# Performance work log

Measured on AMD Instinct MI355X. Metric: run time of the kernel, lower is better.

Reference implementation:

```python
import jax, jax.numpy as jnp
import numpy as np

SCALE = 0.125  # 1/sqrt(D_head=64)
NEG_INF = -1.0e9


def setup_inputs() -> dict:
    key = jax.random.key(0)
    kq, kk, kv, km = jax.random.split(key, 4)
    B, L, N, D = 2, 2048, 16, 64
    query = jax.random.normal(kq, (B, L, N, D), dtype=jnp.float32)
    k = jax.random.normal(kk, (B, L, N, D), dtype=jnp.float32)
    v = jax.random.normal(kv, (B, L, N, D), dtype=jnp.float32)
    attn_mask = jax.random.randint(km, (B, L, L), 0, 2).astype(jnp.bool_)
    return {"query": query, "key": k, "value": v, "attn_mask": attn_mask}


def reference(query, key, value, attn_mask):
    # scores: [B, L_q, L_k, N]
    attention = jnp.einsum('bind,bjnd->bijn', query, key) * SCALE
    # mask broadcast over heads; True positions are masked out
    attention = jnp.where(attn_mask[:, :, :, None], NEG_INF, attention)
    # softmax over the key axis (dim=2), dropout p=0.0 is identity
    attention = jax.nn.softmax(attention, axis=2)
    context = jnp.einsum('bijn,bjnd->bind', attention, value)
    return (context, attention)
```

## Files before the change

### kernel.cpp

```cpp
#include <hip/hip_runtime.h>
#include <hip/hip_bf16.h>

typedef unsigned short u16;
typedef unsigned char u8;
typedef __attribute__((ext_vector_type(8))) short bf16x8;
typedef __attribute__((ext_vector_type(4))) float f32x4;

#define MFMA16(a, b, c) __builtin_amdgcn_mfma_f32_16x16x32_bf16(a, b, c, 0, 0, 0)

static __device__ __forceinline__ u16 f2bf(float f) {
    __hip_bfloat16 h = __float2bfloat16(f);
    return *reinterpret_cast<u16*>(&h);
}
static __device__ __forceinline__ float bf2f(u16 h) {
    unsigned u = ((unsigned)h) << 16;
    return __uint_as_float(u);
}

__global__ __launch_bounds__(256) void kconv_kernel(const float* __restrict__ kf,
                                                    u16* __restrict__ kb) {
    const size_t i = ((size_t)blockIdx.x * 256 + threadIdx.x) * 4;
    float4 f = *(const float4*)(kf + i);
    alignas(8) u16 w[4] = {f2bf(f.x), f2bf(f.y), f2bf(f.z), f2bf(f.w)};
    *(uint2*)(kb + i) = *(const uint2*)w;
}

__global__ __launch_bounds__(256) void vt_kernel(const float* __restrict__ v,
                                                 u16* __restrict__ vt) {
    __shared__ u16 T[64][72];
    const int t = threadIdx.x, bid = blockIdx.x;
    const int b = bid >> 9, n = bid & 15, j0 = ((bid >> 4) & 31) << 6;
    {
        const int jj = t >> 4, tt = t & 15;
#pragma unroll
        for (int rep = 0; rep < 4; rep++) {
            const int j = rep * 16 + jj;
            const float* src = v + (((size_t)((b * 2048 + j0 + j) * 16 + n)) << 6) + tt * 4;
            float4 f = *(const float4*)src;
            alignas(8) u16 w[4] = {f2bf(f.x), f2bf(f.y), f2bf(f.z), f2bf(f.w)};
            *(uint2*)&T[j][tt * 4] = *(const uint2*)w;
        }
    }
    __syncthreads();
    {
        const int d = t >> 2, jq = t & 3;
        alignas(16) u16 w[16];
#pragma unroll
        for (int e = 0; e < 16; e++) w[e] = T[jq * 16 + e][d];
        u16* dst = vt + (((size_t)((b * 16 + n) * 64 + d)) << 11) + j0 + jq * 16;
        *(uint4*)dst = *(const uint4*)&w[0];
        *(uint4*)(dst + 8) = *(const uint4*)&w[8];
    }
}

__global__ __launch_bounds__(1024, 4) void attn_kernel(
    const float* __restrict__ qf, const u16* __restrict__ kb_g,
    const u16* __restrict__ vt, const void* __restrict__ mask,
    float* __restrict__ ctx, float* __restrict__ attn) {
    __shared__ u16 maskT[2048];
    __shared__ u16 pbuf[16][16][40];

    const int tid = threadIdx.x;
    const int lane = tid & 63;
    const int wv = tid >> 6;
    const int g = lane >> 4, c = lane & 15;
    const int rbit = g * 4;

    const int bid = blockIdx.x;
    const int b = ((bid & 7) < 4) ? 0 : 1;
    const int idx = ((bid >> 3) << 2) | (bid & 3);
    const int i0 = idx << 4;

    bool mask_is_u8;
    {
        unsigned acc = 0;
        const unsigned* mw = (const unsigned*)mask;
#pragma unroll
        for (int i = 0; i < 64; i++) acc |= mw[i];
        mask_is_u8 = (acc & 0xFFFFFF00u) != 0u;
    }

    {
        const size_t base = ((size_t)(b * 2048 + i0)) * 2048 + (size_t)tid * 2;
        unsigned m0 = 0, m1 = 0;
        if (mask_is_u8) {
            const u8* m8 = (const u8*)mask;
#pragma unroll
            for (int i = 0; i < 16; i++) {
                const u8* mp = m8 + base + (size_t)i * 2048;
                if (mp[0]) m0 |= (1u << i);
                if (mp[1]) m1 |= (1u << i);
            }
        } else {
            const int* m32 = (const int*)mask;
#pragma unroll
            for (int i = 0; i < 16; i++) {
                const int* mp = m32 + base + (size_t)i * 2048;
                if (mp[0]) m0 |= (1u << i);
                if (mp[1]) m1 |= (1u << i);
            }
        }
        *reinterpret_cast<unsigned*>(&maskT[tid * 2]) = m0 | (m1 << 16);
    }
    __syncthreads();

    bf16x8 aq0, aq1;
    {
        const float* qp = qf + (((size_t)(b * 2048 + i0 + c) * 16 + wv) << 6) + g * 8;
        float4 f0 = *(const float4*)qp;
        float4 f1 = *(const float4*)(qp + 4);
        float4 f2 = *(const float4*)(qp + 32);
        float4 f3 = *(const float4*)(qp + 36);
        alignas(16) u16 w0[8] = {f2bf(f0.x), f2bf(f0.y), f2bf(f0.z), f2bf(f0.w),
                                 f2bf(f1.x), f2bf(f1.y), f2bf(f1.z), f2bf(f1.w)};
        alignas(16) u16 w1[8] = {f2bf(f2.x), f2bf(f2.y), f2bf(f2.z), f2bf(f2.w),
                                 f2bf(f3.x), f2bf(f3.y), f2bf(f3.z), f2bf(f3.w)};
        aq0 = *(const bf16x8*)w0;
        aq1 = *(const bf16x8*)w1;
    }

    const u16* kb = kb_g + (((size_t)(b * 2048) * 16 + wv) << 6) + g * 8;
    const u16* vb = vt + (((size_t)(b * 16 + wv)) << 17);

    float l0 = 0.f, l1 = 0.f, l2 = 0.f, l3 = 0.f;
    for (int j0 = 0; j0 < 2048; j0 += 16) {
        const u16* kp = kb + (size_t)(j0 + c) * 1024;
        bf16x8 b0 = *(const bf16x8*)kp;
        bf16x8 b1 = *(const bf16x8*)(kp + 32);
        f32x4 s = {0.f, 0.f, 0.f, 0.f};
        s = MFMA16(aq0, b0, s);
        s = MFMA16(aq1, b1, s);
        const unsigned mt = maskT[j0 + c];
        l0 += __expf(((mt >> (rbit + 0)) & 1) ? -1e9f : s[0] * 0.125f);
        l1 += __expf(((mt >> (rbit + 1)) & 1) ? -1e9f : s[1] * 0.125f);
        l2 += __expf(((mt >> (rbit + 2)) & 1) ? -1e9f : s[2] * 0.125f);
        l3 += __expf(((mt >> (rbit + 3)) & 1) ? -1e9f : s[3] * 0.125f);
    }
#pragma unroll
    for (int off = 1; off <= 8; off <<= 1) {
        l0 += __shfl_xor(l0, off);
        l1 += __shfl_xor(l1, off);
        l2 += __shfl_xor(l2, off);
        l3 += __shfl_xor(l3, off);
    }
    const float n0i = (l0 != 0.f) ? 1.f / l0 : 0.f;
    const float n1i = (l1 != 0.f) ? 1.f / l1 : 0.f;
    const float n2i = (l2 != 0.f) ? 1.f / l2 : 0.f;
    const float n3i = (l3 != 0.f) ? 1.f / l3 : 0.f;

    f32x4 o0 = {0.f, 0.f, 0.f, 0.f}, o1 = o0, o2 = o0, o3 = o0;

    const int wo_i = tid >> 6;
    const int wo_c = tid & 63;
    const int wo_j = wo_c >> 1;
    const int wo_n = (wo_c & 1) << 3;
    float* attn_row = attn + (((size_t)(b * 2048 + i0 + wo_i)) << 15) + wo_n;

    for (int j0 = 0; j0 < 2048; j0 += 32) {
#pragma unroll
        for (int sub = 0; sub < 2; sub++) {
            const int jb = j0 + (sub << 4);
            const u16* kp = kb + (size_t)(jb + c) * 1024;
            bf16x8 b0 = *(const bf16x8*)kp;
            bf16x8 b1 = *(const bf16x8*)(kp + 32);
            f32x4 s = {0.f, 0.f, 0.f, 0.f};
            s = MFMA16(aq0, b0, s);
            s = MFMA16(aq1, b1, s);
            const unsigned mt = maskT[jb + c];
            const int jj = (sub << 4) + c;
            pbuf[wv][rbit + 0][jj] =
                f2bf(__expf(((mt >> (rbit + 0)) & 1) ? -1e9f : s[0] * 0.125f) * n0i);
            pbuf[wv][rbit + 1][jj] =
                f2bf(__expf(((mt >> (rbit + 1)) & 1) ? -1e9f : s[1] * 0.125f) * n1i);
            pbuf[wv][rbit + 2][jj] =
                f2bf(__expf(((mt >> (rbit + 2)) & 1) ? -1e9f : s[2] * 0.125f) * n2i);
            pbuf[wv][rbit + 3][jj] =
                f2bf(__expf(((mt >> (rbit + 3)) & 1) ? -1e9f : s[3] * 0.125f) * n3i);
        }
        __syncthreads();
        {
            const bf16x8 ap = *(const bf16x8*)&pbuf[wv][c][g * 8];
            const u16* vp = vb + (size_t)c * 2048 + j0 + g * 8;
            bf16x8 v0 = *(const bf16x8*)(vp);
            bf16x8 v1 = *(const bf16x8*)(vp + 16 * 2048);
            bf16x8 v2 = *(const bf16x8*)(vp + 32 * 2048);
            bf16x8 v3 = *(const bf16x8*)(vp + 48 * 2048);
            o0 = MFMA16(ap, v0, o0);
            o1 = MFMA16(ap, v1, o1);
            o2 = MFMA16(ap, v2, o2);
            o3 = MFMA16(ap, v3, o3);
        }
        {
            alignas(16) float w[8];
#pragma unroll
            for (int e = 0; e < 8; e++) w[e] = bf2f(pbuf[wo_n + e][wo_i][wo_j]);
            float* dst = attn_row + (size_t)(j0 + wo_j) * 16;
            *(float4*)dst = *(const float4*)&w[0];
            *(float4*)(dst + 4) = *(const float4*)&w[4];
        }
        __syncthreads();
    }

#pragma unroll
    for (int r = 0; r < 4; r++) {
        float* cp = ctx + (((size_t)(b * 2048 + i0 + rbit + r) * 16 + wv) << 6) + c;
        cp[0]  = o0[r];
        cp[16] = o1[r];
        cp[32] = o2[r];
        cp[48] = o3[r];
    }
}

extern "C" void kernel_launch(void* const* d_in, const int* in_sizes, int n_in,
                              void* d_out, int out_size, void* d_ws, size_t ws_size,
                              hipStream_t stream) {
    const float* q   = (const float*)d_in[0];
    const float* k   = (const float*)d_in[1];
    const float* v   = (const float*)d_in[2];
    const void* mask = (const void*)d_in[3];

    float* ctx  = (float*)d_out;
    float* attn = (float*)d_out + 4194304;

    u16* vt = (u16*)d_ws;
    u16* kb = vt + 4194304;

    kconv_kernel<<<4096, 256, 0, stream>>>(k, kb);
    vt_kernel<<<1024, 256, 0, stream>>>(v, vt);
    attn_kernel<<<256, 1024, 0, stream>>>(q, kb, vt, mask, ctx, attn);
}
```

Baseline: 979.7 us.

## Double-buffer P tile, prefetch next K/V in registers, drop second barrier

The second-pass loop now double-buffers the shared probability tile, so the trailing __syncthreads is removed and one LDS-only barrier remains per iteration. K and V fragments for the next 32-column step are loaded into registers while the current step's PV MFMAs and attention writeback run, hiding global load latency. Attention output stores become nontemporal to avoid polluting cache. It costs extra registers and LDS at 1024 threads per block, which may cause spills or lower occupancy.

Result: faster. 919.2 us (-6.2%).

```diff
diff --git a/kernel.cpp b/kernel.cpp
--- a/kernel.cpp
+++ b/kernel.cpp
@@ -7,6 +7,13 @@
 typedef __attribute__((ext_vector_type(4))) float f32x4;
 
 #define MFMA16(a, b, c) __builtin_amdgcn_mfma_f32_16x16x32_bf16(a, b, c, 0, 0, 0)
+
+#define LGKM_BARRIER()                                     \
+    do {                                                   \
+        asm volatile("s_waitcnt lgkmcnt(0)" ::: "memory"); \
+        __builtin_amdgcn_s_barrier();                      \
+        asm volatile("" ::: "memory");                     \
+    } while (0)
 
 static __device__ __forceinline__ u16 f2bf(float f) {
     __hip_bfloat16 h = __float2bfloat16(f);
@@ -58,7 +65,7 @@
     const u16* __restrict__ vt, const void* __restrict__ mask,
     float* __restrict__ ctx, float* __restrict__ attn) {
     __shared__ u16 maskT[2048];
-    __shared__ u16 pbuf[16][16][40];
+    __shared__ u16 pbuf[2][16][16][40];
 
     const int tid = threadIdx.x;
     const int lane = tid & 63;
@@ -156,49 +163,89 @@
     const int wo_n = (wo_c & 1) << 3;
     float* attn_row = attn + (((size_t)(b * 2048 + i0 + wo_i)) << 15) + wo_n;
 
-    for (int j0 = 0; j0 < 2048; j0 += 32) {
-#pragma unroll
-        for (int sub = 0; sub < 2; sub++) {
-            const int jb = j0 + (sub << 4);
-            const u16* kp = kb + (size_t)(jb + c) * 1024;
-            bf16x8 b0 = *(const bf16x8*)kp;
-            bf16x8 b1 = *(const bf16x8*)(kp + 32);
+    bf16x8 ck0a, ck0b, ck1a, ck1b, cv0, cv1, cv2, cv3;
+    {
+        const u16* kp0 = kb + (size_t)c * 1024;
+        ck0a = *(const bf16x8*)kp0;
+        ck0b = *(const bf16x8*)(kp0 + 32);
+        const u16* kp1 = kb + (size_t)(16 + c) * 1024;
+        ck1a = *(const bf16x8*)kp1;
+        ck1b = *(const bf16x8*)(kp1 + 32);
+        const u16* vp = vb + (size_t)c * 2048 + g * 8;
+        cv0 = *(const bf16x8*)(vp);
+        cv1 = *(const bf16x8*)(vp + 16 * 2048);
+        cv2 = *(const bf16x8*)(vp + 32 * 2048);
+        cv3 = *(const bf16x8*)(vp + 48 * 2048);
+    }
+
+    int p = 0;
+    for (int j0 = 0; j0 < 2048; j0 += 32, p ^= 1) {
+        {
             f32x4 s = {0.f, 0.f, 0.f, 0.f};
-            s = MFMA16(aq0, b0, s);
-            s = MFMA16(aq1, b1, s);
-            const unsigned mt = maskT[jb + c];
-            const int jj = (sub << 4) + c;
-            pbuf[wv][rbit + 0][jj] =
+            s = MFMA16(aq0, ck0a, s);
+            s = MFMA16(aq1, ck0b, s);
+            const unsigned mt = maskT[j0 + c];
+            pbuf[p][wv][rbit + 0][c] =
                 f2bf(__expf(((mt >> (rbit + 0)) & 1) ? -1e9f : s[0] * 0.125f) * n0i);
-            pbuf[wv][rbit + 1][jj] =
+            pbuf[p][wv][rbit + 1][c] =
                 f2bf(__expf(((mt >> (rbit + 1)) & 1) ? -1e9f : s[1] * 0.125f) * n1i);
-            pbuf[wv][rbit + 2][jj] =
+            pbuf[p][wv][rbit + 2][c] =
                 f2bf(__expf(((mt >> (rbit + 2)) & 1) ? -1e9f : s[2] * 0.125f) * n2i);
-            pbuf[wv][rbit + 3][jj] =
+            pbuf[p][wv][rbit + 3][c] =
                 f2bf(__expf(((mt >> (rbit + 3)) & 1) ? -1e9f : s[3] * 0.125f) * n3i);
         }
-        __syncthreads();
-        {
-            const bf16x8 ap = *(const bf16x8*)&pbuf[wv][c][g * 8];
-            const u16* vp = vb + (size_t)c * 2048 + j0 + g * 8;
-            bf16x8 v0 = *(const bf16x8*)(vp);
-            bf16x8 v1 = *(const bf16x8*)(vp + 16 * 2048);
-            bf16x8 v2 = *(const bf16x8*)(vp + 32 * 2048);
-            bf16x8 v3 = *(const bf16x8*)(vp + 48 * 2048);
-            o0 = MFMA16(ap, v0, o0);
-            o1 = MFMA16(ap, v1, o1);
-            o2 = MFMA16(ap, v2, o2);
-            o3 = MFMA16(ap, v3, o3);
-        }
+        {
+            f32x4 s = {0.f, 0.f, 0.f, 0.f};
+            s = MFMA16(aq0, ck1a, s);
+            s = MFMA16(aq1, ck1b, s);
+            const unsigned mt = maskT[j0 + 16 + c];
+            pbuf[p][wv][rbit + 0][16 + c] =
+                f2bf(__expf(((mt >> (rbit + 0)) & 1) ? -1e9f : s[0] * 0.125f) * n0i);
+            pbuf[p][wv][rbit + 1][16 + c] =
+                f2bf(__expf(((mt >> (rbit + 1)) & 1) ? -1e9f : s[1] * 0.125f) * n1i);
+            pbuf[p][wv][rbit + 2][16 + c] =
+                f2bf(__expf(((mt >> (rbit + 2)) & 1) ? -1e9f : s[2] * 0.125f) * n2i);
+            pbuf[p][wv][rbit + 3][16 + c] =
+                f2bf(__expf(((mt >> (rbit + 3)) & 1) ? -1e9f : s[3] * 0.125f) * n3i);
+        }
+        LGKM_BARRIER();
+
+        const bf16x8 ap = *(const bf16x8*)&pbuf[p][wv][c][g * 8];
+
+        const int jn = (j0 + 32) & 2047;
+        bf16x8 nk0a, nk0b, nk1a, nk1b, nv0, nv1, nv2, nv3;
+        {
+            const u16* kp0 = kb + (size_t)(jn + c) * 1024;
+            nk0a = *(const bf16x8*)kp0;
+            nk0b = *(const bf16x8*)(kp0 + 32);
+            const u16* kp1 = kb + (size_t)(jn + 16 + c) * 1024;
+            nk1a = *(const bf16x8*)kp1;
+            nk1b = *(const bf16x8*)(kp1 + 32);
+            const u16* vp = vb + (size_t)c * 2048 + jn + g * 8;
+            nv0 = *(const bf16x8*)(vp);
+            nv1 = *(const bf16x8*)(vp + 16 * 2048);
+            nv2 = *(const bf16x8*)(vp + 32 * 2048);
+            nv3 = *(const bf16x8*)(vp + 48 * 2048);
+        }
+
+        o0 = MFMA16(ap, cv0, o0);
+        o1 = MFMA16(ap, cv1, o1);
+        o2 = MFMA16(ap, cv2, o2);
+        o3 = MFMA16(ap, cv3, o3);
+
+        __builtin_amdgcn_sched_barrier(0);
+
         {
             alignas(16) float w[8];
 #pragma unroll
-            for (int e = 0; e < 8; e++) w[e] = bf2f(pbuf[wo_n + e][wo_i][wo_j]);
+            for (int e = 0; e < 8; e++) w[e] = bf2f(pbuf[p][wo_n + e][wo_i][wo_j]);
             float* dst = attn_row + (size_t)(j0 + wo_j) * 16;
-            *(float4*)dst = *(const float4*)&w[0];
-            *(float4*)(dst + 4) = *(const float4*)&w[4];
-        }
-        __syncthreads();
+            __builtin_nontemporal_store(*(const f32x4*)&w[0], (f32x4*)dst);
+            __builtin_nontemporal_store(*(const f32x4*)&w[4], (f32x4*)(dst + 4));
+        }
+
+        ck0a = nk0a; ck0b = nk0b; ck1a = nk1a; ck1b = nk1b;
+        cv0 = nv0; cv1 = nv1; cv2 = nv2; cv3 = nv3;
     }
 
 #pragma unroll
```

## Software-pipeline K/V register prefetch and double-buffer P tile with single barrier

Applied to the files above, without the earlier changes.

Prefetches K fragments one step ahead in the row-sum pass, and in the main pass keeps two sets of K and V register fragments loaded two steps ahead. The P staging buffer in shared memory is double-buffered, so each 32-column step needs one barrier instead of two. The barrier is issued manually after an LDS wait. The aim is to hide global-load latency behind MFMA and exp work and to cut barrier stalls. In exchange it uses more registers under launch_bounds(1024,4), which could cause spills. With a single barrier, correctness now depends on the two P buffers alternating.

Result: slower. 1.024 ms (+4.6%).

```diff
diff --git a/kernel.cpp b/kernel.cpp
--- a/kernel.cpp
+++ b/kernel.cpp
@@ -7,6 +7,13 @@
 typedef __attribute__((ext_vector_type(4))) float f32x4;
 
 #define MFMA16(a, b, c) __builtin_amdgcn_mfma_f32_16x16x32_bf16(a, b, c, 0, 0, 0)
+
+#define LGKM_BARRIER()                                     \
+    do {                                                   \
+        asm volatile("s_waitcnt lgkmcnt(0)" ::: "memory"); \
+        __builtin_amdgcn_s_barrier();                      \
+        asm volatile("" ::: "memory");                     \
+    } while (0)
 
 static __device__ __forceinline__ u16 f2bf(float f) {
     __hip_bfloat16 h = __float2bfloat16(f);
@@ -53,12 +60,33 @@
     }
 }
 
+#define LOADK(ra, rb, rc2, rd, jb)                            \
+    do {                                                      \
+        const int jw_ = (jb) & 2047;                          \
+        const u16* kp0_ = kb + (size_t)(jw_ + c) * 1024;      \
+        ra = *(const bf16x8*)kp0_;                            \
+        rb = *(const bf16x8*)(kp0_ + 32);                     \
+        const u16* kp1_ = kb + (size_t)(jw_ + 16 + c) * 1024; \
+        rc2 = *(const bf16x8*)kp1_;                           \
+        rd = *(const bf16x8*)(kp1_ + 32);                     \
+    } while (0)
+
+#define LOADV(r0, r1, r2, r3, jb)                             \
+    do {                                                      \
+        const int jw_ = (jb) & 2047;                          \
+        const u16* vp_ = vb + (size_t)c * 2048 + jw_ + g * 8; \
+        r0 = *(const bf16x8*)(vp_);                           \
+        r1 = *(const bf16x8*)(vp_ + 16 * 2048);               \
+        r2 = *(const bf16x8*)(vp_ + 32 * 2048);               \
+        r3 = *(const bf16x8*)(vp_ + 48 * 2048);               \
+    } while (0)
+
 __global__ __launch_bounds__(1024, 4) void attn_kernel(
     const float* __restrict__ qf, const u16* __restrict__ kb_g,
     const u16* __restrict__ vt, const void* __restrict__ mask,
     float* __restrict__ ctx, float* __restrict__ attn) {
     __shared__ u16 maskT[2048];
-    __shared__ u16 pbuf[16][16][40];
+    __shared__ u16 pbuf[2][16][16][40];
 
     const int tid = threadIdx.x;
     const int lane = tid & 63;
@@ -123,18 +151,44 @@
     const u16* vb = vt + (((size_t)(b * 16 + wv)) << 17);
 
     float l0 = 0.f, l1 = 0.f, l2 = 0.f, l3 = 0.f;
-    for (int j0 = 0; j0 < 2048; j0 += 16) {
-        const u16* kp = kb + (size_t)(j0 + c) * 1024;
-        bf16x8 b0 = *(const bf16x8*)kp;
-        bf16x8 b1 = *(const bf16x8*)(kp + 32);
-        f32x4 s = {0.f, 0.f, 0.f, 0.f};
-        s = MFMA16(aq0, b0, s);
-        s = MFMA16(aq1, b1, s);
-        const unsigned mt = maskT[j0 + c];
-        l0 += __expf(((mt >> (rbit + 0)) & 1) ? -1e9f : s[0] * 0.125f);
-        l1 += __expf(((mt >> (rbit + 1)) & 1) ? -1e9f : s[1] * 0.125f);
-        l2 += __expf(((mt >> (rbit + 2)) & 1) ? -1e9f : s[2] * 0.125f);
-        l3 += __expf(((mt >> (rbit + 3)) & 1) ? -1e9f : s[3] * 0.125f);
+    bf16x8 pa0, pa1, pb0, pb1;
+    {
+        const u16* kp = kb + (size_t)c * 1024;
+        pa0 = *(const bf16x8*)kp;
+        pa1 = *(const bf16x8*)(kp + 32);
+        const u16* kq = kb + (size_t)(16 + c) * 1024;
+        pb0 = *(const bf16x8*)kq;
+        pb1 = *(const bf16x8*)(kq + 32);
+    }
+    for (int j0 = 0; j0 < 2048; j0 += 32) {
+        {
+            f32x4 s = {0.f, 0.f, 0.f, 0.f};
+            s = MFMA16(aq0, pa0, s);
+            s = MFMA16(aq1, pa1, s);
+            const int jw = (j0 + 32) & 2047;
+            const u16* kp = kb + (size_t)(jw + c) * 1024;
+            pa0 = *(const bf16x8*)kp;
+            pa1 = *(const bf16x8*)(kp + 32);
+            const unsigned mt = maskT[j0 + c];
+            l0 += __expf(((mt >> (rbit + 0)) & 1) ? -1e9f : s[0] * 0.125f);
+            l1 += __expf(((mt >> (rbit + 1)) & 1) ? -1e9f : s[1] * 0.125f);
+            l2 += __expf(((mt >> (rbit + 2)) & 1) ? -1e9f : s[2] * 0.125f);
+            l3 += __expf(((mt >> (rbit + 3)) & 1) ? -1e9f : s[3] * 0.125f);
+        }
+        {
+            f32x4 s = {0.f, 0.f, 0.f, 0.f};
+            s = MFMA16(aq0, pb0, s);
+            s = MFMA16(aq1, pb1, s);
+            const int jw = (j0 + 48) & 2047;
+            const u16* kq = kb + (size_t)(jw + c) * 1024;
+            pb0 = *(const bf16x8*)kq;
+            pb1 = *(const bf16x8*)(kq + 32);
+            const unsigned mt = maskT[j0 + 16 + c];
+            l0 += __expf(((mt >> (rbit + 0)) & 1) ? -1e9f : s[0] * 0.125f);
+            l1 += __expf(((mt >> (rbit + 1)) & 1) ? -1e9f : s[1] * 0.125f);
+            l2 += __expf(((mt >> (rbit + 2)) & 1) ? -1e9f : s[2] * 0.125f);
+            l3 += __expf(((mt >> (rbit + 3)) & 1) ? -1e9f : s[3] * 0.125f);
+        }
     }
 #pragma unroll
     for (int off = 1; off <= 8; off <<= 1) {
@@ -156,50 +210,69 @@
     const int wo_n = (wo_c & 1) << 3;
     float* attn_row = attn + (((size_t)(b * 2048 + i0 + wo_i)) << 15) + wo_n;
 
-    for (int j0 = 0; j0 < 2048; j0 += 32) {
-#pragma unroll
-        for (int sub = 0; sub < 2; sub++) {
-            const int jb = j0 + (sub << 4);
-            const u16* kp = kb + (size_t)(jb + c) * 1024;
-            bf16x8 b0 = *(const bf16x8*)kp;
-            bf16x8 b1 = *(const bf16x8*)(kp + 32);
-            f32x4 s = {0.f, 0.f, 0.f, 0.f};
-            s = MFMA16(aq0, b0, s);
-            s = MFMA16(aq1, b1, s);
-            const unsigned mt = maskT[jb + c];
-            const int jj = (sub << 4) + c;
-            pbuf[wv][rbit + 0][jj] =
-                f2bf(__expf(((mt >> (rbit + 0)) & 1) ? -1e9f : s[0] * 0.125f) * n0i);
-            pbuf[wv][rbit + 1][jj] =
-                f2bf(__expf(((mt >> (rbit + 1)) & 1) ? -1e9f : s[1] * 0.125f) * n1i);
-            pbuf[wv][rbit + 2][jj] =
-                f2bf(__expf(((mt >> (rbit + 2)) & 1) ? -1e9f : s[2] * 0.125f) * n2i);
-            pbuf[wv][rbit + 3][jj] =
-                f2bf(__expf(((mt >> (rbit + 3)) & 1) ? -1e9f : s[3] * 0.125f) * n3i);
-        }
-        __syncthreads();
-        {
-            const bf16x8 ap = *(const bf16x8*)&pbuf[wv][c][g * 8];
-            const u16* vp = vb + (size_t)c * 2048 + j0 + g * 8;
-            bf16x8 v0 = *(const bf16x8*)(vp);
-            bf16x8 v1 = *(const bf16x8*)(vp + 16 * 2048);
-            bf16x8 v2 = *(const bf16x8*)(vp + 32 * 2048);
-            bf16x8 v3 = *(const bf16x8*)(vp + 48 * 2048);
-            o0 = MFMA16(ap, v0, o0);
-            o1 = MFMA16(ap, v1, o1);
-            o2 = MFMA16(ap, v2, o2);
-            o3 = MFMA16(ap, v3, o3);
-        }
-        {
-            alignas(16) float w[8];
-#pragma unroll
-            for (int e = 0; e < 8; e++) w[e] = bf2f(pbuf[wo_n + e][wo_i][wo_j]);
-            float* dst = attn_row + (size_t)(j0 + wo_j) * 16;
-            *(float4*)dst = *(const float4*)&w[0];
-            *(float4*)(dst + 4) = *(const float4*)&w[4];
-        }
-        __syncthreads();
-    }
+#define HALF(pp, KA, KB, KC, KD, Va, Vb, Vc, Vd, jcur)                                 \
+    do {                                                                               \
+        {                                                                              \
+            f32x4 s = {0.f, 0.f, 0.f, 0.f};                                            \
+            s = MFMA16(aq0, KA, s);                                                    \
+            s = MFMA16(aq1, KB, s);                                                    \
+            const unsigned mt = maskT[(jcur) + c];                                     \
+            pbuf[pp][wv][rbit + 0][c] =                                                \
+                f2bf(__expf(((mt >> (rbit + 0)) & 1) ? -1e9f : s[0] * 0.125f) * n0i);  \
+            pbuf[pp][wv][rbit + 1][c] =                                                \
+                f2bf(__expf(((mt >> (rbit + 1)) & 1) ? -1e9f : s[1] * 0.125f) * n1i);  \
+            pbuf[pp][wv][rbit + 2][c] =                                                \
+                f2bf(__expf(((mt >> (rbit + 2)) & 1) ? -1e9f : s[2] * 0.125f) * n2i);  \
+            pbuf[pp][wv][rbit + 3][c] =                                                \
+                f2bf(__expf(((mt >> (rbit + 3)) & 1) ? -1e9f : s[3] * 0.125f) * n3i);  \
+        }                                                                              \
+        {                                                                              \
+            f32x4 s = {0.f, 0.f, 0.f, 0.f};                                            \
+            s = MFMA16(aq0, KC, s);                                                    \
+            s = MFMA16(aq1, KD, s);                                                    \
+            const unsigned mt = maskT[(jcur) + 16 + c];                                \
+            pbuf[pp][wv][rbit + 0][16 + c] =                                           \
+                f2bf(__expf(((mt >> (rbit + 0)) & 1) ? -1e9f : s[0] * 0.125f) * n0i);  \
+            pbuf[pp][wv][rbit + 1][16 + c] =                                           \
+                f2bf(__expf(((mt >> (rbit + 1)) & 1) ? -1e9f : s[1] * 0.125f) * n1i);  \
+            pbuf[pp][wv][rbit + 2][16 + c] =                                           \
+                f2bf(__expf(((mt >> (rbit + 2)) & 1) ? -1e9f : s[2] * 0.125f) * n2i);  \
+            pbuf[pp][wv][rbit + 3][16 + c] =                                           \
+                f2bf(__expf(((mt >> (rbit + 3)) & 1) ? -1e9f : s[3] * 0.125f) * n3i);  \
+        }                                                                              \
+        LOADK(KA, KB, KC, KD, (jcur) + 64);                                            \
+        LGKM_BARRIER();                                                                \
+        {                                                                              \
+            const bf16x8 ap_ = *(const bf16x8*)&pbuf[pp][wv][c][g * 8];                \
+            o0 = MFMA16(ap_, Va, o0);                                                  \
+            o1 = MFMA16(ap_, Vb, o1);                                                  \
+            o2 = MFMA16(ap_, Vc, o2);                                                  \
+            o3 = MFMA16(ap_, Vd, o3);                                                  \
+        }                                                                              \
+        LOADV(Va, Vb, Vc, Vd, (jcur) + 64);                                            \
+        __builtin_amdgcn_sched_barrier(0);                                             \
+        {                                                                              \
+            alignas(16) float w[8];                                                    \
+            _Pragma("unroll") for (int e = 0; e < 8; e++)                              \
+                w[e] = bf2f(pbuf[pp][wo_n + e][wo_i][wo_j]);                           \
+            float* dst = attn_row + (size_t)((jcur) + wo_j) * 16;                      \
+            *(f32x4*)dst = *(const f32x4*)&w[0];                                       \
+            *(f32x4*)(dst + 4) = *(const f32x4*)&w[4];                                 \
+        }                                                                              \
+    } while (0)
+
+    bf16x8 K0a, K0b, K0c, K0d, V00, V01, V02, V03;
+    bf16x8 K1a, K1b, K1c, K1d, V10, V11, V12, V13;
+    LOADK(K0a, K0b, K0c, K0d, 0);
+    LOADV(V00, V01, V02, V03, 0);
+    LOADK(K1a, K1b, K1c, K1d, 32);
+    LOADV(V10, V11, V12, V13, 32);
+
+    for (int j0 = 0; j0 < 2048; j0 += 64) {
+        HALF(0, K0a, K0b, K0c, K0d, V00, V01, V02, V03, j0);
+        HALF(1, K1a, K1b, K1c, K1d, V10, V11, V12, V13, j0 + 32);
+    }
+#undef HALF
 
 #pragma unroll
     for (int r = 0; r < 4; r++) {
```
